# Kernel optimization log

Hardware: AMD Instinct MI355X
Metric: run time of the kernel (lower is better)

## Reference

```python
import jax, jax.numpy as jnp
import numpy as np

# NF4 (NormalFloat4) codebook from QLoRA / bitsandbytes
NF4_TABLE = jnp.array([
    -1.0, -0.6961928009986877, -0.5250730514526367, -0.39491748809814453,
    -0.28444138169288635, -0.18477343022823334, -0.09105003625154495, 0.0,
    0.07958029955625534, 0.16093020141124725, 0.24611230194568634,
    0.33791524171829224, 0.44070982933044434, 0.5626170039176941,
    0.7229568362236023, 1.0], dtype=jnp.float32)

IN_FEATURES = 4096
OUT_FEATURES = 11008
BLOCKSIZE = 64
NUMEL = IN_FEATURES * OUT_FEATURES          # 45_088_768
PACKED = NUMEL // 2                          # 22_544_384
NBLOCKS = NUMEL // BLOCKSIZE                 # 704_512


def setup_inputs() -> dict:
    key = jax.random.key(0)
    k1, k2, k3, k4 = jax.random.split(key, 4)
    x = jax.random.normal(k1, (2048, IN_FEATURES), dtype=jnp.float32)
    # packed uint8 codes, stored as int32 in [0, 256)
    packed = jax.random.randint(k2, (PACKED,), 0, 256, dtype=jnp.int32)
    # per-block absmax scales (positive)
    absmax = jax.random.uniform(k3, (NBLOCKS,), dtype=jnp.float32, minval=0.01, maxval=1.0)
    bias = jax.random.normal(k4, (OUT_FEATURES,), dtype=jnp.float32)
    return {"x": x, "packed": packed, "absmax": absmax, "bias": bias}


def _dequantize_nf4(packed, absmax):
    # unpack two 4-bit codes per byte: high nibble first, then low nibble
    hi = packed >> 4            # [P]
    lo = packed & 0xF           # [P]
    codes = jnp.stack([hi, lo], axis=-1).reshape(-1)       # [numel]
    vals = jnp.take(NF4_TABLE, codes)                      # [numel]
    # per-block absmax scaling
    w = (vals.reshape(-1, BLOCKSIZE) * absmax[:, None]).reshape(OUT_FEATURES, IN_FEATURES)
    return w


def reference(x, packed, absmax, bias):
    w = _dequantize_nf4(packed, absmax)                    # [out, in]
    # y = x @ W^T + b
    return jnp.einsum('ti,oi->to', x, w) + bias[None, :]
```

## Files before the change

### kernel.cpp

```cpp
#include <hip/hip_runtime.h>
#include <hip/hip_bf16.h>


#define IN_F   4096
#define OUT_F  11008
#define M_ROWS 2048
#define BM 128
#define BN 128
#define BK 64
#define LDSS 72

typedef short  s16x8 __attribute__((ext_vector_type(8)));
typedef unsigned short u16x8 __attribute__((ext_vector_type(8)));
typedef float  f32x4 __attribute__((ext_vector_type(4)));
typedef int    i32x4 __attribute__((ext_vector_type(4)));
typedef unsigned int u32x4 __attribute__((ext_vector_type(4)));

__device__ const float NF4_C[16] = {
    -1.0f, -0.6961928009986877f, -0.5250730514526367f, -0.39491748809814453f,
    -0.28444138169288635f, -0.18477343022823334f, -0.09105003625154495f, 0.0f,
    0.07958029955625534f, 0.16093020141124725f, 0.24611230194568634f,
    0.33791524171829224f, 0.44070982933044434f, 0.5626170039176941f,
    0.7229568362236023f, 1.0f};

static __device__ __forceinline__ unsigned short f2bf(float f) {
    union { float f; unsigned int u; } c;
    c.f = f;
    unsigned int u = c.u;
    u += 0x7fffu + ((u >> 16) & 1u);
    return (unsigned short)(u >> 16);
}

static __device__ __forceinline__ void gload_lds16(const void* g, void* l) {
    __builtin_amdgcn_global_load_lds(
        (const __attribute__((address_space(1))) void*)g,
        (__attribute__((address_space(3))) void*)l, 16, 0, 0);
}

#define DQ_BLOCKS 11008
#define CV_BLOCKS 4096

__global__ __launch_bounds__(256)
void prep_kernel(const float* __restrict__ x,
                 const int* __restrict__ packed,
                 const float* __restrict__ absmax,
                 unsigned short* __restrict__ xb,
                 unsigned short* __restrict__ wb) {
    if (blockIdx.x < DQ_BLOCKS) {
        __shared__ float tab_hi[256];
        __shared__ float tab_lo[256];
        tab_hi[threadIdx.x] = NF4_C[threadIdx.x >> 4];
        tab_lo[threadIdx.x] = NF4_C[threadIdx.x & 15];
        __syncthreads();

        const size_t u0 = (size_t)blockIdx.x * 512 + threadIdx.x;
#pragma unroll
        for (int h = 0; h < 2; ++h) {
            const size_t u = u0 + h * 256;
            i32x4 v = __builtin_nontemporal_load(
                reinterpret_cast<const i32x4*>(packed) + u);
            const float s = absmax[u >> 3];
            unsigned int ow[4];
#pragma unroll
            for (int j = 0; j < 4; ++j) {
                const int b = v[j] & 0xFF;
                ow[j] = (unsigned int)f2bf(tab_hi[b] * s)
                      | ((unsigned int)f2bf(tab_lo[b] * s) << 16);
            }
            *(reinterpret_cast<u32x4*>(wb) + u) = (u32x4){ow[0], ow[1], ow[2], ow[3]};
        }
    } else {
        const size_t u0 = (size_t)(blockIdx.x - DQ_BLOCKS) * 512 + threadIdx.x;
#pragma unroll
        for (int h = 0; h < 2; ++h) {
            const size_t u = u0 + h * 256;
            f32x4 v = __builtin_nontemporal_load(
                reinterpret_cast<const f32x4*>(x) + u);
            ushort4 o;
            o.x = f2bf(v[0]); o.y = f2bf(v[1]); o.z = f2bf(v[2]); o.w = f2bf(v[3]);
            *(reinterpret_cast<ushort4*>(xb) + u) = o;
        }
    }
}

__global__ __launch_bounds__(256, 2)
void gemm_bt_kernel(const unsigned short* __restrict__ xb,
                    const unsigned short* __restrict__ wb,
                    const float* __restrict__ bias,
                    float* __restrict__ out) {
    __shared__ __align__(16) unsigned short As[BM * BK];
    __shared__ __align__(16) unsigned short Bs[BN * BK];

    const int tid  = threadIdx.x;
    const int lane = tid & 63;
    const int wave = tid >> 6;
    const int quad = lane >> 4;
    const int l16  = lane & 15;
    const int wm = wave & 1;
    const int wn = wave >> 1;

    const int mBase = blockIdx.x * BM;
    const int nBase = blockIdx.y * BN;

    const int srow = tid >> 3;
    const int sc   = tid & 7;
    const int scS  = sc ^ (srow & 7);

    f32x4 acc[4][4];
#pragma unroll
    for (int mi = 0; mi < 4; ++mi)
#pragma unroll
        for (int ni = 0; ni < 4; ++ni)
            acc[mi][ni] = (f32x4){0.f, 0.f, 0.f, 0.f};

    const unsigned short* aSrc = xb + (size_t)(mBase + srow) * IN_F + scS * 8;
    const unsigned short* bSrc = wb + (size_t)(nBase + srow) * IN_F + scS * 8;

    const int sw = l16 & 7;

    for (int kt = 0; kt < IN_F / BK; ++kt) {
        const int k0 = kt * BK;
        __syncthreads();
#pragma unroll
        for (int i = 0; i < 4; ++i)
            gload_lds16(aSrc + (size_t)i * 32 * IN_F + k0, &As[(i * 32 + srow) * BK + sc * 8]);
#pragma unroll
        for (int i = 0; i < 4; ++i)
            gload_lds16(bSrc + (size_t)i * 32 * IN_F + k0, &Bs[(i * 32 + srow) * BK + sc * 8]);
        __syncthreads();

#pragma unroll
        for (int kk = 0; kk < 2; ++kk) {
            const int q  = kk * 4 + quad;
            const int rd = (q ^ sw) * 8;
            s16x8 af[4], bfr[4];
#pragma unroll
            for (int mi = 0; mi < 4; ++mi)
                af[mi] = *reinterpret_cast<const s16x8*>(
                    &As[(wm * 64 + mi * 16 + l16) * BK + rd]);
#pragma unroll
            for (int ni = 0; ni < 4; ++ni)
                bfr[ni] = *reinterpret_cast<const s16x8*>(
                    &Bs[(wn * 64 + ni * 16 + l16) * BK + rd]);
#pragma unroll
            for (int mi = 0; mi < 4; ++mi)
#pragma unroll
                for (int ni = 0; ni < 4; ++ni)
                    acc[mi][ni] = __builtin_amdgcn_mfma_f32_16x16x32_bf16(
                        af[mi], bfr[ni], acc[mi][ni], 0, 0, 0);
        }
    }

    float bv[4];
#pragma unroll
    for (int ni = 0; ni < 4; ++ni)
        bv[ni] = bias[nBase + wn * 64 + ni * 16 + l16];
#pragma unroll
    for (int mi = 0; mi < 4; ++mi) {
        const int rbase = mBase + wm * 64 + mi * 16 + quad * 4;
#pragma unroll
        for (int ni = 0; ni < 4; ++ni) {
            const int col = nBase + wn * 64 + ni * 16 + l16;
#pragma unroll
            for (int r = 0; r < 4; ++r)
                __builtin_nontemporal_store(acc[mi][ni][r] + bv[ni],
                    &out[(size_t)(rbase + r) * OUT_F + col]);
        }
    }
}

__global__ __launch_bounds__(256, 2)
void nf4_linear_fused(const float* __restrict__ x,
                      const int* __restrict__ packed,
                      const float* __restrict__ absmax,
                      const float* __restrict__ bias,
                      float* __restrict__ out) {
    __shared__ __align__(16) unsigned short As[BM * LDSS];
    __shared__ __align__(16) unsigned short Bs[BN * LDSS];
    __shared__ float2 tab[256];

    const int tid  = threadIdx.x;
    const int lane = tid & 63;
    const int wave = tid >> 6;
    const int quad = lane >> 4;
    const int l16  = lane & 15;
    const int wm = wave & 1;
    const int wn = wave >> 1;
    const int mBase = blockIdx.y * BM;
    const int nBase = blockIdx.x * BN;

    tab[tid] = make_float2(NF4_C[tid >> 4], NF4_C[tid & 15]);

    f32x4 acc[4][4];
#pragma unroll
    for (int mi = 0; mi < 4; ++mi)
#pragma unroll
        for (int ni = 0; ni < 4; ++ni)
            acc[mi][ni] = (f32x4){0.f, 0.f, 0.f, 0.f};

    const int brow  = tid >> 1;
    const int bhalf = tid & 1;
    const int ng    = nBase + brow;

    for (int kt = 0; kt < IN_F / BK; ++kt) {
        const int k0 = kt * BK;
        __syncthreads();
#pragma unroll
        for (int i = 0; i < 4; ++i) {
            int gid = tid + i * 256;
            int row = gid >> 3;
            int c8  = gid & 7;
            const float4* src = reinterpret_cast<const float4*>(
                x + (size_t)(mBase + row) * IN_F + k0 + c8 * 8);
            float4 v0 = src[0];
            float4 v1 = src[1];
            u16x8 o;
            o[0] = f2bf(v0.x); o[1] = f2bf(v0.y); o[2] = f2bf(v0.z); o[3] = f2bf(v0.w);
            o[4] = f2bf(v1.x); o[5] = f2bf(v1.y); o[6] = f2bf(v1.z); o[7] = f2bf(v1.w);
            *reinterpret_cast<u16x8*>(&As[row * LDSS + c8 * 8]) = o;
        }
        {
            const float scale = absmax[(size_t)ng * 64 + (k0 >> 6)];
            const int4* bp = reinterpret_cast<const int4*>(
                packed + (size_t)ng * (IN_F / 2) + (k0 >> 1) + bhalf * 16);
            const int colw = bhalf * 32;
#pragma unroll
            for (int c = 0; c < 4; ++c) {
                int4 v = bp[c];
                int vs[4] = {v.x, v.y, v.z, v.w};
                unsigned int ow[4];
#pragma unroll
                for (int j = 0; j < 4; ++j) {
                    float2 t = tab[vs[j] & 0xFF];
                    ow[j] = (unsigned int)f2bf(t.x * scale)
                          | ((unsigned int)f2bf(t.y * scale) << 16);
                }
                *reinterpret_cast<uint4*>(&Bs[brow * LDSS + colw + c * 8]) =
                    *reinterpret_cast<const uint4*>(ow);
            }
        }
        __syncthreads();

#pragma unroll
        for (int kk = 0; kk < 2; ++kk) {
            const int kof = kk * 32 + quad * 8;
            s16x8 af[4], bfr[4];
#pragma unroll
            for (int mi = 0; mi < 4; ++mi)
                af[mi] = *reinterpret_cast<const s16x8*>(
                    &As[(wm * 64 + mi * 16 + l16) * LDSS + kof]);
#pragma unroll
            for (int ni = 0; ni < 4; ++ni)
                bfr[ni] = *reinterpret_cast<const s16x8*>(
                    &Bs[(wn * 64 + ni * 16 + l16) * LDSS + kof]);
#pragma unroll
            for (int mi = 0; mi < 4; ++mi)
#pragma unroll
                for (int ni = 0; ni < 4; ++ni)
                    acc[mi][ni] = __builtin_amdgcn_mfma_f32_16x16x32_bf16(
                        af[mi], bfr[ni], acc[mi][ni], 0, 0, 0);
        }
    }

    float bv[4];
#pragma unroll
    for (int ni = 0; ni < 4; ++ni)
        bv[ni] = bias[nBase + wn * 64 + ni * 16 + l16];
#pragma unroll
    for (int mi = 0; mi < 4; ++mi) {
        const int rbase = mBase + wm * 64 + mi * 16 + quad * 4;
#pragma unroll
        for (int ni = 0; ni < 4; ++ni) {
            const int col = nBase + wn * 64 + ni * 16 + l16;
#pragma unroll
            for (int r = 0; r < 4; ++r)
                out[(size_t)(rbase + r) * OUT_F + col] = acc[mi][ni][r] + bv[ni];
        }
    }
}

extern "C" void kernel_launch(void* const* d_in, const int* in_sizes, int n_in,
                              void* d_out, int out_size, void* d_ws, size_t ws_size,
                              hipStream_t stream) {
    const float* x      = (const float*)d_in[0];
    const int*   packed = (const int*)d_in[1];
    const float* absmax = (const float*)d_in[2];
    const float* bias   = (const float*)d_in[3];
    float* out = (float*)d_out;

    const size_t xb_bytes = (size_t)M_ROWS * IN_F * 2;
    const size_t wb_bytes = (size_t)OUT_F * IN_F * 2;
    if (ws_size >= xb_bytes + wb_bytes) {
        unsigned short* xb = (unsigned short*)d_ws;
        unsigned short* wb = (unsigned short*)((char*)d_ws + xb_bytes);
        prep_kernel<<<dim3(DQ_BLOCKS + CV_BLOCKS), dim3(256), 0, stream>>>(
            x, packed, absmax, xb, wb);
        gemm_bt_kernel<<<dim3(M_ROWS / BM, OUT_F / BN), dim3(256), 0, stream>>>(
            xb, wb, bias, out);
    } else {
        nf4_linear_fused<<<dim3(OUT_F / BN, M_ROWS / BM), dim3(256), 0, stream>>>(
            x, packed, absmax, bias, out);
    }
}
```

Measured before the change: 358.2 us.

## Replace GEMM with double-buffered 512-thread 128x256 tile kernel with MFMA phase scheduling

Replaces the bf16 GEMM with a kernel of 8 waves and a 128x256 block tile. It double-buffers the LDS tiles so the next K-tile's global-to-LDS loads overlap the current MFMAs, using vmcnt waits instead of two full syncthreads per iteration. The inner loop is split into phases with s_barrier, setprio and sched_barrier to interleave LDS reads with MFMA bursts across waves. The cost is higher LDS use (96KB per block) and more barriers, so occupancy may drop. Because 11008/256 = 43, the grid has 16x43 blocks, fewer than before.

```diff
diff --git a/kernel.cpp b/kernel.cpp
--- a/kernel.cpp
+++ b/kernel.cpp
@@ -6,8 +6,9 @@
 #define OUT_F  11008
 #define M_ROWS 2048
 #define BM 128
-#define BN 128
+#define BN 256
 #define BK 64
+#define NT (IN_F / BK)
 #define LDSS 72
 
 typedef short  s16x8 __attribute__((ext_vector_type(8)));
@@ -83,13 +84,127 @@
     }
 }
 
+__global__ __launch_bounds__(512, 2)
+void gemm_8ph_kernel(const unsigned short* __restrict__ xb,
+                     const unsigned short* __restrict__ wb,
+                     const float* __restrict__ bias,
+                     float* __restrict__ out) {
+    __shared__ __align__(16) unsigned short As[2][BM * BK];
+    __shared__ __align__(16) unsigned short Bs[2][BN * BK];
+
+    const int tid  = threadIdx.x;
+    const int lane = tid & 63;
+    const int wave = tid >> 6;
+    const int quad = lane >> 4;
+    const int l16  = lane & 15;
+    const int wm = wave >> 2;
+    const int wn = wave & 3;
+
+    const int mBase = blockIdx.x * BM;
+    const int nBase = blockIdx.y * BN;
+
+    const int srow = tid >> 3;
+    const int sc   = tid & 7;
+    const int scS  = sc ^ (srow & 7);
+
+    const unsigned short* aSrc = xb + (size_t)(mBase + srow) * IN_F + scS * 8;
+    const unsigned short* bSrc = wb + (size_t)(nBase + srow) * IN_F + scS * 8;
+    const int dstOff = srow * BK + sc * 8;
+
+#define STAGE_TILE(T, BSEL) do {                                               \
+        const int k0_ = (T) * BK;                                              \
+        unsigned short* Ad_ = &As[(BSEL)][0];                                  \
+        unsigned short* Bd_ = &Bs[(BSEL)][0];                                  \
+        gload_lds16(aSrc + k0_,                      Ad_ + dstOff);            \
+        gload_lds16(aSrc + (size_t)64 * IN_F + k0_,  Ad_ + 64 * BK + dstOff);  \
+        gload_lds16(bSrc + k0_,                      Bd_ + dstOff);            \
+        gload_lds16(bSrc + (size_t)64 * IN_F + k0_,  Bd_ + 64 * BK + dstOff);  \
+        gload_lds16(bSrc + (size_t)128 * IN_F + k0_, Bd_ + 128 * BK + dstOff); \
+        gload_lds16(bSrc + (size_t)192 * IN_F + k0_, Bd_ + 192 * BK + dstOff); \
+    } while (0)
+
+    f32x4 acc[4][4];
+#pragma unroll
+    for (int mi = 0; mi < 4; ++mi)
+#pragma unroll
+        for (int ni = 0; ni < 4; ++ni)
+            acc[mi][ni] = (f32x4){0.f, 0.f, 0.f, 0.f};
+
+    const int sw  = l16 & 7;
+    const int rd0 = (quad ^ sw) * 8;
+    const int rd1 = ((4 + quad) ^ sw) * 8;
+    const int aRow = (wm * 64 + l16) * BK;
+    const int bRow = (wn * 64 + l16) * BK;
+
+    STAGE_TILE(0, 0);
+
+    for (int t = 0; t < NT; ++t) {
+        const int b = t & 1;
+        if (t + 1 < NT) {
+            STAGE_TILE(t + 1, b ^ 1);
+            asm volatile("s_waitcnt vmcnt(6)" ::: "memory");
+        } else {
+            asm volatile("s_waitcnt vmcnt(0)" ::: "memory");
+        }
+        __builtin_amdgcn_s_barrier();
+
+        const unsigned short* Ab = &As[b][0];
+        const unsigned short* Bb = &Bs[b][0];
+
+        s16x8 af[4][2];
+#pragma unroll
+        for (int mi = 0; mi < 4; ++mi) {
+            af[mi][0] = *reinterpret_cast<const s16x8*>(&Ab[aRow + mi * 16 * BK + rd0]);
+            af[mi][1] = *reinterpret_cast<const s16x8*>(&Ab[aRow + mi * 16 * BK + rd1]);
+        }
+#pragma unroll
+        for (int q = 0; q < 4; ++q) {
+            s16x8 b0 = *reinterpret_cast<const s16x8*>(&Bb[bRow + q * 16 * BK + rd0]);
+            s16x8 b1 = *reinterpret_cast<const s16x8*>(&Bb[bRow + q * 16 * BK + rd1]);
+            __builtin_amdgcn_s_barrier();
+            asm volatile("s_waitcnt lgkmcnt(0)" ::: "memory");
+            __builtin_amdgcn_sched_barrier(0);
+            __builtin_amdgcn_s_setprio(1);
+#pragma unroll
+            for (int mi = 0; mi < 4; ++mi) {
+                acc[mi][q] = __builtin_amdgcn_mfma_f32_16x16x32_bf16(
+                    af[mi][0], b0, acc[mi][q], 0, 0, 0);
+                acc[mi][q] = __builtin_amdgcn_mfma_f32_16x16x32_bf16(
+                    af[mi][1], b1, acc[mi][q], 0, 0, 0);
+            }
+            __builtin_amdgcn_s_setprio(0);
+            __builtin_amdgcn_s_barrier();
+        }
+    }
+#undef STAGE_TILE
+
+    float bv[4];
+#pragma unroll
+    for (int ni = 0; ni < 4; ++ni)
+        bv[ni] = bias[nBase + wn * 64 + ni * 16 + l16];
+#pragma unroll
+    for (int mi = 0; mi < 4; ++mi) {
+        const int rbase = mBase + wm * 64 + mi * 16 + quad * 4;
+#pragma unroll
+        for (int ni = 0; ni < 4; ++ni) {
+            const int col = nBase + wn * 64 + ni * 16 + l16;
+#pragma unroll
+            for (int r = 0; r < 4; ++r)
+                __builtin_nontemporal_store(acc[mi][ni][r] + bv[ni],
+                    &out[(size_t)(rbase + r) * OUT_F + col]);
+        }
+    }
+}
+
 __global__ __launch_bounds__(256, 2)
-void gemm_bt_kernel(const unsigned short* __restrict__ xb,
-                    const unsigned short* __restrict__ wb,
-                    const float* __restrict__ bias,
-                    float* __restrict__ out) {
-    __shared__ __align__(16) unsigned short As[BM * BK];
-    __shared__ __align__(16) unsigned short Bs[BN * BK];
+void nf4_linear_fused(const float* __restrict__ x,
+                      const int* __restrict__ packed,
+                      const float* __restrict__ absmax,
+                      const float* __restrict__ bias,
+                      float* __restrict__ out) {
+    __shared__ __align__(16) unsigned short As[128 * LDSS];
+    __shared__ __align__(16) unsigned short Bs[128 * LDSS];
+    __shared__ float2 tab[256];
 
     const int tid  = threadIdx.x;
     const int lane = tid & 63;
@@ -98,96 +213,8 @@
     const int l16  = lane & 15;
     const int wm = wave & 1;
     const int wn = wave >> 1;
-
-    const int mBase = blockIdx.x * BM;
-    const int nBase = blockIdx.y * BN;
-
-    const int srow = tid >> 3;
-    const int sc   = tid & 7;
-    const int scS  = sc ^ (srow & 7);
-
-    f32x4 acc[4][4];
-#pragma unroll
-    for (int mi = 0; mi < 4; ++mi)
-#pragma unroll
-        for (int ni = 0; ni < 4; ++ni)
-            acc[mi][ni] = (f32x4){0.f, 0.f, 0.f, 0.f};
-
-    const unsigned short* aSrc = xb + (size_t)(mBase + srow) * IN_F + scS * 8;
-    const unsigned short* bSrc = wb + (size_t)(nBase + srow) * IN_F + scS * 8;
-
-    const int sw = l16 & 7;
-
-    for (int kt = 0; kt < IN_F / BK; ++kt) {
-        const int k0 = kt * BK;
-        __syncthreads();
-#pragma unroll
-        for (int i = 0; i < 4; ++i)
-            gload_lds16(aSrc + (size_t)i * 32 * IN_F + k0, &As[(i * 32 + srow) * BK + sc * 8]);
-#pragma unroll
-        for (int i = 0; i < 4; ++i)
-            gload_lds16(bSrc + (size_t)i * 32 * IN_F + k0, &Bs[(i * 32 + srow) * BK + sc * 8]);
-        __syncthreads();
-
-#pragma unroll
-        for (int kk = 0; kk < 2; ++kk) {
-            const int q  = kk * 4 + quad;
-            const int rd = (q ^ sw) * 8;
-            s16x8 af[4], bfr[4];
-#pragma unroll
-            for (int mi = 0; mi < 4; ++mi)
-                af[mi] = *reinterpret_cast<const s16x8*>(
-                    &As[(wm * 64 + mi * 16 + l16) * BK + rd]);
-#pragma unroll
-            for (int ni = 0; ni < 4; ++ni)
-                bfr[ni] = *reinterpret_cast<const s16x8*>(
-                    &Bs[(wn * 64 + ni * 16 + l16) * BK + rd]);
-#pragma unroll
-            for (int mi = 0; mi < 4; ++mi)
-#pragma unroll
-                for (int ni = 0; ni < 4; ++ni)
-                    acc[mi][ni] = __builtin_amdgcn_mfma_f32_16x16x32_bf16(
-                        af[mi], bfr[ni], acc[mi][ni], 0, 0, 0);
-        }
-    }
-
-    float bv[4];
-#pragma unroll
-    for (int ni = 0; ni < 4; ++ni)
-        bv[ni] = bias[nBase + wn * 64 + ni * 16 + l16];
-#pragma unroll
-    for (int mi = 0; mi < 4; ++mi) {
-        const int rbase = mBase + wm * 64 + mi * 16 + quad * 4;
-#pragma unroll
-        for (int ni = 0; ni < 4; ++ni) {
-            const int col = nBase + wn * 64 + ni * 16 + l16;
-#pragma unroll
-            for (int r = 0; r < 4; ++r)
-                __builtin_nontemporal_store(acc[mi][ni][r] + bv[ni],
-                    &out[(size_t)(rbase + r) * OUT_F + col]);
-        }
-    }
-}
-
-__global__ __launch_bounds__(256, 2)
-void nf4_linear_fused(const float* __restrict__ x,
-                      const int* __restrict__ packed,
-                      const float* __restrict__ absmax,
-                      const float* __restrict__ bias,
-                      float* __restrict__ out) {
-    __shared__ __align__(16) unsigned short As[BM * LDSS];
-    __shared__ __align__(16) unsigned short Bs[BN * LDSS];
-    __shared__ float2 tab[256];
-
-    const int tid  = threadIdx.x;
-    const int lane = tid & 63;
-    const int wave = tid >> 6;
-    const int quad = lane >> 4;
-    const int l16  = lane & 15;
-    const int wm = wave & 1;
-    const int wn = wave >> 1;
-    const int mBase = blockIdx.y * BM;
-    const int nBase = blockIdx.x * BN;
+    const int mBase = blockIdx.y * 128;
+    const int nBase = blockIdx.x * 128;
 
     tab[tid] = make_float2(NF4_C[tid >> 4], NF4_C[tid & 15]);
 
@@ -295,10 +322,10 @@
         unsigned short* wb = (unsigned short*)((char*)d_ws + xb_bytes);
         prep_kernel<<<dim3(DQ_BLOCKS + CV_BLOCKS), dim3(256), 0, stream>>>(
             x, packed, absmax, xb, wb);
-        gemm_bt_kernel<<<dim3(M_ROWS / BM, OUT_F / BN), dim3(256), 0, stream>>>(
+        gemm_8ph_kernel<<<dim3(M_ROWS / BM, OUT_F / BN), dim3(512), 0, stream>>>(
             xb, wb, bias, out);
     } else {
-        nf4_linear_fused<<<dim3(OUT_F / BN, M_ROWS / BM), dim3(256), 0, stream>>>(
+        nf4_linear_fused<<<dim3(OUT_F / 128, M_ROWS / 128), dim3(256), 0, stream>>>(
             x, packed, absmax, bias, out);
     }
 }
```

Result: slower. 476.1 us (+32.9%).
